# Kernel optimization log

Hardware: AMD Instinct MI355X
Metric: run time of the kernel (lower is better)

The kernel has to match this reference:

```python
import jax, jax.numpy as jnp
import numpy as np

D_MODEL = 768
NUM_HEADS = 12
D_K = D_MODEL // NUM_HEADS


def setup_inputs() -> dict:
    key = jax.random.key(0)
    ks = jax.random.split(key, 11)
    B, L = 1, 4096
    s = 1.0 / np.sqrt(D_MODEL)
    return {
        "q": jax.random.normal(ks[0], (B, L, D_MODEL), jnp.float32),
        "k": jax.random.normal(ks[1], (B, L, D_MODEL), jnp.float32),
        "v": jax.random.normal(ks[2], (B, L, D_MODEL), jnp.float32),
        "Wq": jax.random.normal(ks[3], (D_MODEL, D_MODEL), jnp.float32) * s,
        "bq": jax.random.normal(ks[4], (D_MODEL,), jnp.float32) * s,
        "Wk": jax.random.normal(ks[5], (D_MODEL, D_MODEL), jnp.float32) * s,
        "bk": jax.random.normal(ks[6], (D_MODEL,), jnp.float32) * s,
        "Wv": jax.random.normal(ks[7], (D_MODEL, D_MODEL), jnp.float32) * s,
        "bv": jax.random.normal(ks[8], (D_MODEL,), jnp.float32) * s,
        "Wo": jax.random.normal(ks[9], (D_MODEL, D_MODEL), jnp.float32) * s,
        "bo": jax.random.normal(ks[10], (D_MODEL,), jnp.float32) * s,
    }


def reference(q, k, v, Wq, bq, Wk, bk, Wv, bv, Wo, bo):
    B, L, _ = q.shape
    # linear projections (torch Linear: x @ W.T + b)
    qp = q @ Wq.T + bq
    kp = k @ Wk.T + bk
    vp = v @ Wv.T + bv
    # split heads: (B, H, L, d_k)
    def split(x):
        return x.reshape(B, L, NUM_HEADS, D_K).transpose(0, 2, 1, 3)
    qh, kh, vh = split(qp), split(kp), split(vp)
    scale = 1.0 / jnp.sqrt(jnp.asarray(D_K, qh.dtype))
    scores = jnp.einsum("bhqd,bhkd->bhqk", qh, kh) * scale  # (B,H,L,L)
    weights = jax.nn.softmax(scores, axis=-1)
    out = jnp.einsum("bhqk,bhkd->bhqd", weights, vh)
    out = out.transpose(0, 2, 1, 3).reshape(B, L, D_MODEL)
    return out @ Wo.T + bo
```

## Files before the change

### kernel.cpp

```cpp
#include <hip/hip_runtime.h>
#include <stdint.h>
#include <math.h>

#define L_SEQ  4096
#define DMODEL 768
#define NHEADS 12
#define DKH    64
#define QSCALE 0.18033688011112042f

typedef _Float16 f16;
typedef __attribute__((ext_vector_type(8))) _Float16 half8;
typedef __attribute__((ext_vector_type(4))) _Float16 half4;
typedef __attribute__((ext_vector_type(4))) float f32x4;
typedef __attribute__((ext_vector_type(16))) float f32x16;
typedef __attribute__((ext_vector_type(4))) unsigned int uint4v;

#define MFMA16(a, b, c) __builtin_amdgcn_mfma_f32_16x16x32_f16(a, b, c, 0, 0, 0)
#define MFMA32(a, b, c) __builtin_amdgcn_mfma_f32_32x32x16_f16(a, b, c, 0, 0, 0)

#define NE ((size_t)L_SEQ * DMODEL)
#define WE ((size_t)DMODEL * DMODEL)

static __device__ __forceinline__ unsigned int pack2(float a, float b) {
  return __builtin_bit_cast(unsigned int, __builtin_amdgcn_cvt_pkrtz(a, b));
}

__global__ __launch_bounds__(256)
void cvt_all(const float* __restrict__ q, const float* __restrict__ k,
             const float* __restrict__ v, const float* __restrict__ Wq,
             const float* __restrict__ Wk, const float* __restrict__ Wv,
             const float* __restrict__ Wo, f16* __restrict__ x16,
             f16* __restrict__ w16)
{
  const size_t NE4 = NE / 4, WE4 = WE / 4;
  size_t i = (size_t)blockIdx.x * 256 + threadIdx.x;
  const float* srcs[7] = {q, k, v, Wq, Wk, Wv, Wo};
  f16* dsts[7] = {x16, x16 + NE, x16 + 2 * NE,
                  w16, w16 + WE, w16 + 2 * WE, w16 + 3 * WE};
  const size_t sz4[7] = {NE4, NE4, NE4, WE4, WE4, WE4, WE4};
  int r = 0; size_t off = i;
  while (off >= sz4[r]) { off -= sz4[r]; ++r; }
  float4 f = reinterpret_cast<const float4*>(srcs[r])[off];
  half4 h; h[0] = (f16)f.x; h[1] = (f16)f.y; h[2] = (f16)f.z; h[3] = (f16)f.w;
  reinterpret_cast<half4*>(dsts[r])[off] = h;
}

template<int KIND>
__global__ __launch_bounds__(256)
void gemm_big(const f16* __restrict__ Abase, const f16* __restrict__ Wbase,
              const float* __restrict__ bq, const float* __restrict__ bk,
              const float* __restrict__ bv,
              f16* __restrict__ Qp, f16* __restrict__ Kp, f16* __restrict__ VpT,
              float* __restrict__ Ofp)
{
  __shared__ f16 As[128][72];
  __shared__ f16 Bs[128][72];
  const int tid  = threadIdx.x;
  const int lane = tid & 63, wid = tid >> 6;
  const int l31  = lane & 31, hc = lane >> 5;
  const int wm   = (wid & 1) * 64, wn = (wid >> 1) * 64;
  const int m0   = blockIdx.y * 128;

  int widx, n0;
  const f16 *A, *W;
  if (KIND == 0) {
    widx = blockIdx.x / 6;
    n0   = (blockIdx.x % 6) * 128;
    A = Abase + (size_t)widx * NE;
    W = Wbase + (size_t)widx * WE;
  } else {
    widx = 3;
    n0   = blockIdx.x * 128;
    A = Abase;
    W = Wbase;
  }

  const int srow = tid >> 1, sseg = (tid & 1) * 32;
  const f16* aptr = A + (size_t)(m0 + srow) * DMODEL + sseg;
  const f16* bptr = W + (size_t)(n0 + srow) * DMODEL + sseg;

  half8 ar[4], br[4];
#pragma unroll
  for (int t = 0; t < 4; ++t) {
    ar[t] = *reinterpret_cast<const half8*>(aptr + t * 8);
    br[t] = *reinterpret_cast<const half8*>(bptr + t * 8);
  }

  f32x16 acc[2][2] = {};

  for (int k0 = 0; k0 < DMODEL; k0 += 64) {
#pragma unroll
    for (int t = 0; t < 4; ++t) {
      *reinterpret_cast<half8*>(&As[srow][sseg + t * 8]) = ar[t];
      *reinterpret_cast<half8*>(&Bs[srow][sseg + t * 8]) = br[t];
    }
    __syncthreads();

    if (k0 + 64 < DMODEL) {
#pragma unroll
      for (int t = 0; t < 4; ++t) {
        ar[t] = *reinterpret_cast<const half8*>(aptr + k0 + 64 + t * 8);
        br[t] = *reinterpret_cast<const half8*>(bptr + k0 + 64 + t * 8);
      }
    }

#pragma unroll
    for (int s = 0; s < 4; ++s) {
      half8 af[2], bf[2];
#pragma unroll
      for (int a = 0; a < 2; ++a)
        af[a] = *reinterpret_cast<half8*>(&As[wm + a * 32 + l31][s * 16 + hc * 8]);
#pragma unroll
      for (int b = 0; b < 2; ++b)
        bf[b] = *reinterpret_cast<half8*>(&Bs[wn + b * 32 + l31][s * 16 + hc * 8]);
#pragma unroll
      for (int a = 0; a < 2; ++a)
#pragma unroll
        for (int b = 0; b < 2; ++b)
          acc[a][b] = MFMA32(af[a], bf[b], acc[a][b]);
    }
    __syncthreads();
  }

#pragma unroll
  for (int b = 0; b < 2; ++b) {
    const int gn = n0 + wn + b * 32 + l31;
    float bias;
    if (KIND == 0) bias = (widx == 0) ? bq[gn] : (widx == 1) ? bk[gn] : bv[gn];
    else           bias = bq[gn];
#pragma unroll
    for (int a = 0; a < 2; ++a) {
      const int gmb = m0 + wm + a * 32 + 4 * hc;
      if (KIND == 1) {
#pragma unroll
        for (int r = 0; r < 16; ++r) {
          const int gm = gmb + (r & 3) + 8 * (r >> 2);
          Ofp[(size_t)gm * DMODEL + gn] = acc[a][b][r] + bias;
        }
      } else if (widx == 2) {
#pragma unroll
        for (int g = 0; g < 4; ++g) {
          half4 o4;
#pragma unroll
          for (int t = 0; t < 4; ++t) o4[t] = (f16)(acc[a][b][4 * g + t] + bias);
          *reinterpret_cast<half4*>(VpT + (size_t)gn * L_SEQ + gmb + 8 * g) = o4;
        }
      } else if (widx == 0) {
#pragma unroll
        for (int r = 0; r < 16; ++r) {
          const int gm = gmb + (r & 3) + 8 * (r >> 2);
          Qp[(size_t)gm * DMODEL + gn] = (f16)((acc[a][b][r] + bias) * QSCALE);
        }
      } else {
#pragma unroll
        for (int r = 0; r < 16; ++r) {
          const int gm = gmb + (r & 3) + 8 * (r >> 2);
          Kp[(size_t)gm * DMODEL + gn] = (f16)(acc[a][b][r] + bias);
        }
      }
    }
  }
}

__global__ __launch_bounds__(256, 3)
void attn_mfma4(const f16* __restrict__ Qp, const f16* __restrict__ Kp,
                const f16* __restrict__ VpT, f16* __restrict__ AO)
{
  const int h  = blockIdx.x;
  const int q0 = blockIdx.y * 64;
  const int tid  = threadIdx.x;
  const int lane = tid & 63, wid = tid >> 6;
  const int l31  = lane & 31, hc = lane >> 5;
  const int qh   = wid & 1, kh = wid >> 1;

  __shared__ __align__(16) char smem[25088];
  f16 (*Ks)[72] = (f16 (*)[72])smem;
  f16 (*Vt)[72] = (f16 (*)[72])(smem + 9216);
  float* Of  = (float*)smem;
  float* lf  = (float*)(smem + 16384);
  f16*   Of16 = (f16*)(smem + 16640);

  half8 qf[4];
#pragma unroll
  for (int st = 0; st < 4; ++st)
    qf[st] = *reinterpret_cast<const half8*>(
        Qp + (size_t)(q0 + qh * 32 + l31) * DMODEL + h * DKH + st * 16 + hc * 8);

  f32x16 oacc[2] = {};
  float lsum = 0.0f;

  const int srow = tid >> 2, sseg = (tid & 3) * 16;
  const f16* kbase = Kp  + (size_t)srow * DMODEL + h * DKH + sseg;
  const f16* vbase = VpT + (size_t)(h * DKH + srow) * L_SEQ + sseg;

  half8 k0 = *reinterpret_cast<const half8*>(kbase);
  half8 k1 = *reinterpret_cast<const half8*>(kbase + 8);
  half8 v0 = *reinterpret_cast<const half8*>(vbase);
  half8 v1 = *reinterpret_cast<const half8*>(vbase + 8);

  for (int kt = 0; kt < L_SEQ; kt += 64) {
    *reinterpret_cast<half8*>(&Ks[srow][sseg])     = k0;
    *reinterpret_cast<half8*>(&Ks[srow][sseg + 8]) = k1;
    *reinterpret_cast<half8*>(&Vt[srow][sseg])     = v0;
    *reinterpret_cast<half8*>(&Vt[srow][sseg + 8]) = v1;
    __syncthreads();

    if (kt + 64 < L_SEQ) {
      const f16* kn = kbase + (size_t)(kt + 64) * DMODEL;
      const f16* vn = vbase + (kt + 64);
      k0 = *reinterpret_cast<const half8*>(kn);
      k1 = *reinterpret_cast<const half8*>(kn + 8);
      v0 = *reinterpret_cast<const half8*>(vn);
      v1 = *reinterpret_cast<const half8*>(vn + 8);
    }

    f32x16 s = {};
#pragma unroll
    for (int st = 0; st < 4; ++st) {
      half8 kf = *reinterpret_cast<half8*>(&Ks[kh * 32 + l31][st * 16 + hc * 8]);
      s = MFMA32(kf, qf[st], s);
    }

    unsigned int pk[8];
#pragma unroll
    for (int i = 0; i < 8; ++i) {
      float p0 = exp2f(s[2 * i]);
      float p1 = exp2f(s[2 * i + 1]);
      lsum += p0 + p1;
      pk[i] = pack2(p0, p1);
    }

    unsigned int recv[4];
#pragma unroll
    for (int j = 0; j < 4; ++j) {
      unsigned int sv = hc ? pk[(j & 1) + 4 * (j >> 1)]
                           : pk[2 + (j & 1) + 4 * (j >> 1)];
      recv[j] = (unsigned int)__shfl_xor((int)sv, 32);
    }

#pragma unroll
    for (int st = 0; st < 2; ++st) {
      uint4v pw;
#pragma unroll
      for (int t = 0; t < 4; ++t) {
        unsigned int h0v = (t < 2) ? pk[(t & 1) + 4 * st] : recv[2 * st + (t & 1)];
        unsigned int h1v = (t < 2) ? recv[2 * st + (t & 1)] : pk[(t & 1) + 4 * st + 2];
        pw[t] = hc ? h1v : h0v;
      }
      half8 pf = __builtin_bit_cast(half8, pw);
#pragma unroll
      for (int a = 0; a < 2; ++a) {
        half8 vf = *reinterpret_cast<half8*>(&Vt[a * 32 + l31][kh * 32 + st * 16 + hc * 8]);
        oacc[a] = MFMA32(vf, pf, oacc[a]);
      }
    }
    __syncthreads();
  }

  float lw = lsum + __shfl_xor(lsum, 32);

  if (kh == 0) {
#pragma unroll
    for (int a = 0; a < 2; ++a)
#pragma unroll
      for (int r = 0; r < 16; ++r) {
        int d = a * 32 + (r & 3) + 8 * (r >> 2) + 4 * hc;
        Of[((qh * 64) + d) * 32 + l31] = oacc[a][r];
      }
    if (lane < 32) lf[qh * 32 + l31] = lw;
  }
  __syncthreads();
  if (kh == 1) {
    const float inv = 1.0f / (lf[qh * 32 + l31] + lw);
#pragma unroll
    for (int a = 0; a < 2; ++a)
#pragma unroll
      for (int r = 0; r < 16; ++r) {
        int d = a * 32 + (r & 3) + 8 * (r >> 2) + 4 * hc;
        float val = (Of[((qh * 64) + d) * 32 + l31] + oacc[a][r]) * inv;
        Of16[(qh * 32 + l31) * 64 + d] = (f16)val;
      }
  }
  __syncthreads();

  *reinterpret_cast<half8*>(AO + (size_t)(q0 + srow) * DMODEL + h * DKH + sseg) =
      *reinterpret_cast<half8*>(&Of16[srow * 64 + sseg]);
  *reinterpret_cast<half8*>(AO + (size_t)(q0 + srow) * DMODEL + h * DKH + sseg + 8) =
      *reinterpret_cast<half8*>(&Of16[srow * 64 + sseg + 8]);
}

extern "C" void kernel_launch(void* const* d_in, const int* in_sizes, int n_in,
                              void* d_out, int out_size, void* d_ws, size_t ws_size,
                              hipStream_t stream) {
  const float* q  = (const float*)d_in[0];
  const float* k  = (const float*)d_in[1];
  const float* v  = (const float*)d_in[2];
  const float* Wq = (const float*)d_in[3];
  const float* bq = (const float*)d_in[4];
  const float* Wk = (const float*)d_in[5];
  const float* bk = (const float*)d_in[6];
  const float* Wv = (const float*)d_in[7];
  const float* bv = (const float*)d_in[8];
  const float* Wo = (const float*)d_in[9];
  const float* bo = (const float*)d_in[10];
  float* out = (float*)d_out;

  f16* x16 = (f16*)d_ws;
  f16* w16 = x16 + 3 * NE;
  f16* Qp  = w16 + 4 * WE;
  f16* Kp  = Qp + NE;
  f16* VpT = Kp + NE;
  f16* AO  = VpT + NE;

  const int ncvt = (int)((3 * (NE / 4) + 4 * (WE / 4)) / 256);
  cvt_all<<<ncvt, 256, 0, stream>>>(q, k, v, Wq, Wk, Wv, Wo, x16, w16);

  dim3 gqkv(18, L_SEQ / 128);
  gemm_big<0><<<gqkv, 256, 0, stream>>>(x16, w16, bq, bk, bv,
                                        Qp, Kp, VpT, nullptr);

  dim3 gattn(NHEADS, L_SEQ / 64);
  attn_mfma4<<<gattn, 256, 0, stream>>>(Qp, Kp, VpT, AO);

  dim3 gout(DMODEL / 128, L_SEQ / 128);
  gemm_big<1><<<gout, 256, 0, stream>>>(AO, w16 + 3 * WE, bo, nullptr, nullptr,
                                        nullptr, nullptr, nullptr, out);
}
```

Measured before the change: 249.0 us.

## Split attention keys across four waves and halve GEMM M-tile

The attention kernel grows to 512 threads with 8 waves, so each pair of query waves splits every 128-key tile four ways. Partial outputs and row sums are reduced serially through shared memory. The projection GEMMs use 64x128 tiles instead of 128x128, which doubles the block count for better CU occupancy. The trade-offs are extra reduction sync phases, more shared memory per attention block, and less operand reuse per GEMM block.

Measured after the change: 459.6 us. 84.6% more time.

```diff
diff --git a/kernel.cpp b/kernel.cpp
--- a/kernel.cpp
+++ b/kernel.cpp
@@ -11,11 +11,9 @@
 typedef _Float16 f16;
 typedef __attribute__((ext_vector_type(8))) _Float16 half8;
 typedef __attribute__((ext_vector_type(4))) _Float16 half4;
-typedef __attribute__((ext_vector_type(4))) float f32x4;
 typedef __attribute__((ext_vector_type(16))) float f32x16;
 typedef __attribute__((ext_vector_type(4))) unsigned int uint4v;
 
-#define MFMA16(a, b, c) __builtin_amdgcn_mfma_f32_16x16x32_f16(a, b, c, 0, 0, 0)
 #define MFMA32(a, b, c) __builtin_amdgcn_mfma_f32_32x32x16_f16(a, b, c, 0, 0, 0)
 
 #define NE ((size_t)L_SEQ * DMODEL)
@@ -47,19 +45,19 @@
 
 template<int KIND>
 __global__ __launch_bounds__(256)
-void gemm_big(const f16* __restrict__ Abase, const f16* __restrict__ Wbase,
-              const float* __restrict__ bq, const float* __restrict__ bk,
-              const float* __restrict__ bv,
-              f16* __restrict__ Qp, f16* __restrict__ Kp, f16* __restrict__ VpT,
-              float* __restrict__ Ofp)
+void gemm_t(const f16* __restrict__ Abase, const f16* __restrict__ Wbase,
+            const float* __restrict__ bq, const float* __restrict__ bk,
+            const float* __restrict__ bv,
+            f16* __restrict__ Qp, f16* __restrict__ Kp, f16* __restrict__ VpT,
+            float* __restrict__ Ofp)
 {
-  __shared__ f16 As[128][72];
+  __shared__ f16 As[64][72];
   __shared__ f16 Bs[128][72];
   const int tid  = threadIdx.x;
   const int lane = tid & 63, wid = tid >> 6;
   const int l31  = lane & 31, hc = lane >> 5;
-  const int wm   = (wid & 1) * 64, wn = (wid >> 1) * 64;
-  const int m0   = blockIdx.y * 128;
+  const int wm   = (wid & 1) * 32, wn = (wid >> 1) * 64;
+  const int m0   = blockIdx.y * 64;
 
   int widx, n0;
   const f16 *A, *W;
@@ -75,49 +73,47 @@
     W = Wbase;
   }
 
-  const int srow = tid >> 1, sseg = (tid & 1) * 32;
-  const f16* aptr = A + (size_t)(m0 + srow) * DMODEL + sseg;
-  const f16* bptr = W + (size_t)(n0 + srow) * DMODEL + sseg;
-
-  half8 ar[4], br[4];
-#pragma unroll
-  for (int t = 0; t < 4; ++t) {
-    ar[t] = *reinterpret_cast<const half8*>(aptr + t * 8);
-    br[t] = *reinterpret_cast<const half8*>(bptr + t * 8);
-  }
-
-  f32x16 acc[2][2] = {};
+  const int arow = tid >> 2, aseg = (tid & 3) * 16;
+  const int brow = tid >> 1, bseg = (tid & 1) * 32;
+  const f16* aptr = A + (size_t)(m0 + arow) * DMODEL + aseg;
+  const f16* bptr = W + (size_t)(n0 + brow) * DMODEL + bseg;
+
+  half8 ar[2], br[4];
+#pragma unroll
+  for (int t = 0; t < 2; ++t) ar[t] = *reinterpret_cast<const half8*>(aptr + t * 8);
+#pragma unroll
+  for (int t = 0; t < 4; ++t) br[t] = *reinterpret_cast<const half8*>(bptr + t * 8);
+
+  f32x16 acc[2] = {};
 
   for (int k0 = 0; k0 < DMODEL; k0 += 64) {
 #pragma unroll
-    for (int t = 0; t < 4; ++t) {
-      *reinterpret_cast<half8*>(&As[srow][sseg + t * 8]) = ar[t];
-      *reinterpret_cast<half8*>(&Bs[srow][sseg + t * 8]) = br[t];
-    }
+    for (int t = 0; t < 2; ++t)
+      *reinterpret_cast<half8*>(&As[arow][aseg + t * 8]) = ar[t];
+#pragma unroll
+    for (int t = 0; t < 4; ++t)
+      *reinterpret_cast<half8*>(&Bs[brow][bseg + t * 8]) = br[t];
     __syncthreads();
 
     if (k0 + 64 < DMODEL) {
 #pragma unroll
-      for (int t = 0; t < 4; ++t) {
+      for (int t = 0; t < 2; ++t)
         ar[t] = *reinterpret_cast<const half8*>(aptr + k0 + 64 + t * 8);
+#pragma unroll
+      for (int t = 0; t < 4; ++t)
         br[t] = *reinterpret_cast<const half8*>(bptr + k0 + 64 + t * 8);
-      }
     }
 
 #pragma unroll
     for (int s = 0; s < 4; ++s) {
-      half8 af[2], bf[2];
-#pragma unroll
-      for (int a = 0; a < 2; ++a)
-        af[a] = *reinterpret_cast<half8*>(&As[wm + a * 32 + l31][s * 16 + hc * 8]);
+      half8 af = *reinterpret_cast<half8*>(&As[wm + l31][s * 16 + hc * 8]);
+      half8 bf[2];
 #pragma unroll
       for (int b = 0; b < 2; ++b)
         bf[b] = *reinterpret_cast<half8*>(&Bs[wn + b * 32 + l31][s * 16 + hc * 8]);
 #pragma unroll
-      for (int a = 0; a < 2; ++a)
-#pragma unroll
-        for (int b = 0; b < 2; ++b)
-          acc[a][b] = MFMA32(af[a], bf[b], acc[a][b]);
+      for (int b = 0; b < 2; ++b)
+        acc[b] = MFMA32(af, bf[b], acc[b]);
     }
     __syncthreads();
   }
@@ -128,42 +124,39 @@
     float bias;
     if (KIND == 0) bias = (widx == 0) ? bq[gn] : (widx == 1) ? bk[gn] : bv[gn];
     else           bias = bq[gn];
-#pragma unroll
-    for (int a = 0; a < 2; ++a) {
-      const int gmb = m0 + wm + a * 32 + 4 * hc;
-      if (KIND == 1) {
-#pragma unroll
-        for (int r = 0; r < 16; ++r) {
-          const int gm = gmb + (r & 3) + 8 * (r >> 2);
-          Ofp[(size_t)gm * DMODEL + gn] = acc[a][b][r] + bias;
-        }
-      } else if (widx == 2) {
-#pragma unroll
-        for (int g = 0; g < 4; ++g) {
-          half4 o4;
-#pragma unroll
-          for (int t = 0; t < 4; ++t) o4[t] = (f16)(acc[a][b][4 * g + t] + bias);
-          *reinterpret_cast<half4*>(VpT + (size_t)gn * L_SEQ + gmb + 8 * g) = o4;
-        }
-      } else if (widx == 0) {
-#pragma unroll
-        for (int r = 0; r < 16; ++r) {
-          const int gm = gmb + (r & 3) + 8 * (r >> 2);
-          Qp[(size_t)gm * DMODEL + gn] = (f16)((acc[a][b][r] + bias) * QSCALE);
-        }
-      } else {
-#pragma unroll
-        for (int r = 0; r < 16; ++r) {
-          const int gm = gmb + (r & 3) + 8 * (r >> 2);
-          Kp[(size_t)gm * DMODEL + gn] = (f16)(acc[a][b][r] + bias);
-        }
-      }
-    }
-  }
-}
-
-__global__ __launch_bounds__(256, 3)
-void attn_mfma4(const f16* __restrict__ Qp, const f16* __restrict__ Kp,
+    const int gmb = m0 + wm + 4 * hc;
+    if (KIND == 1) {
+#pragma unroll
+      for (int r = 0; r < 16; ++r) {
+        const int gm = gmb + (r & 3) + 8 * (r >> 2);
+        Ofp[(size_t)gm * DMODEL + gn] = acc[b][r] + bias;
+      }
+    } else if (widx == 2) {
+#pragma unroll
+      for (int g = 0; g < 4; ++g) {
+        half4 o4;
+#pragma unroll
+        for (int t = 0; t < 4; ++t) o4[t] = (f16)(acc[b][4 * g + t] + bias);
+        *reinterpret_cast<half4*>(VpT + (size_t)gn * L_SEQ + gmb + 8 * g) = o4;
+      }
+    } else if (widx == 0) {
+#pragma unroll
+      for (int r = 0; r < 16; ++r) {
+        const int gm = gmb + (r & 3) + 8 * (r >> 2);
+        Qp[(size_t)gm * DMODEL + gn] = (f16)((acc[b][r] + bias) * QSCALE);
+      }
+    } else {
+#pragma unroll
+      for (int r = 0; r < 16; ++r) {
+        const int gm = gmb + (r & 3) + 8 * (r >> 2);
+        Kp[(size_t)gm * DMODEL + gn] = (f16)(acc[b][r] + bias);
+      }
+    }
+  }
+}
+
+__global__ __launch_bounds__(512, 6)
+void attn_mfma5(const f16* __restrict__ Qp, const f16* __restrict__ Kp,
                 const f16* __restrict__ VpT, f16* __restrict__ AO)
 {
   const int h  = blockIdx.x;
@@ -171,13 +164,13 @@
   const int tid  = threadIdx.x;
   const int lane = tid & 63, wid = tid >> 6;
   const int l31  = lane & 31, hc = lane >> 5;
-  const int qh   = wid & 1, kh = wid >> 1;
-
-  __shared__ __align__(16) char smem[25088];
-  f16 (*Ks)[72] = (f16 (*)[72])smem;
-  f16 (*Vt)[72] = (f16 (*)[72])(smem + 9216);
-  float* Of  = (float*)smem;
-  float* lf  = (float*)(smem + 16384);
+  const int qh   = wid & 1, kq = wid >> 1;
+
+  __shared__ __align__(16) char smem[35840];
+  f16 (*Ks)[72]  = (f16 (*)[72])smem;
+  f16 (*Vt)[136] = (f16 (*)[136])(smem + 18432);
+  float* Of   = (float*)smem;
+  float* lf   = (float*)(smem + 16384);
   f16*   Of16 = (f16*)(smem + 16640);
 
   half8 qf[4];
@@ -189,25 +182,26 @@
   f32x16 oacc[2] = {};
   float lsum = 0.0f;
 
-  const int srow = tid >> 2, sseg = (tid & 3) * 16;
-  const f16* kbase = Kp  + (size_t)srow * DMODEL + h * DKH + sseg;
-  const f16* vbase = VpT + (size_t)(h * DKH + srow) * L_SEQ + sseg;
+  const int krow = tid >> 2, kseg = (tid & 3) * 16;
+  const int vrow = tid >> 3, vseg = (tid & 7) * 16;
+  const f16* kbase = Kp  + (size_t)krow * DMODEL + h * DKH + kseg;
+  const f16* vbase = VpT + (size_t)(h * DKH + vrow) * L_SEQ + vseg;
 
   half8 k0 = *reinterpret_cast<const half8*>(kbase);
   half8 k1 = *reinterpret_cast<const half8*>(kbase + 8);
   half8 v0 = *reinterpret_cast<const half8*>(vbase);
   half8 v1 = *reinterpret_cast<const half8*>(vbase + 8);
 
-  for (int kt = 0; kt < L_SEQ; kt += 64) {
-    *reinterpret_cast<half8*>(&Ks[srow][sseg])     = k0;
-    *reinterpret_cast<half8*>(&Ks[srow][sseg + 8]) = k1;
-    *reinterpret_cast<half8*>(&Vt[srow][sseg])     = v0;
-    *reinterpret_cast<half8*>(&Vt[srow][sseg + 8]) = v1;
-    __syncthreads();
-
-    if (kt + 64 < L_SEQ) {
-      const f16* kn = kbase + (size_t)(kt + 64) * DMODEL;
-      const f16* vn = vbase + (kt + 64);
+  for (int kt = 0; kt < L_SEQ; kt += 128) {
+    *reinterpret_cast<half8*>(&Ks[krow][kseg])     = k0;
+    *reinterpret_cast<half8*>(&Ks[krow][kseg + 8]) = k1;
+    *reinterpret_cast<half8*>(&Vt[vrow][vseg])     = v0;
+    *reinterpret_cast<half8*>(&Vt[vrow][vseg + 8]) = v1;
+    __syncthreads();
+
+    if (kt + 128 < L_SEQ) {
+      const f16* kn = kbase + (size_t)(kt + 128) * DMODEL;
+      const f16* vn = vbase + (kt + 128);
       k0 = *reinterpret_cast<const half8*>(kn);
       k1 = *reinterpret_cast<const half8*>(kn + 8);
       v0 = *reinterpret_cast<const half8*>(vn);
@@ -217,7 +211,7 @@
     f32x16 s = {};
 #pragma unroll
     for (int st = 0; st < 4; ++st) {
-      half8 kf = *reinterpret_cast<half8*>(&Ks[kh * 32 + l31][st * 16 + hc * 8]);
+      half8 kf = *reinterpret_cast<half8*>(&Ks[kq * 32 + l31][st * 16 + hc * 8]);
       s = MFMA32(kf, qf[st], s);
     }
 
@@ -250,7 +244,8 @@
       half8 pf = __builtin_bit_cast(half8, pw);
 #pragma unroll
       for (int a = 0; a < 2; ++a) {
-        half8 vf = *reinterpret_cast<half8*>(&Vt[a * 32 + l31][kh * 32 + st * 16 + hc * 8]);
+        half8 vf = *reinterpret_cast<half8*>(
+            &Vt[a * 32 + l31][kq * 32 + st * 16 + hc * 8]);
         oacc[a] = MFMA32(vf, pf, oacc[a]);
       }
     }
@@ -259,7 +254,7 @@
 
   float lw = lsum + __shfl_xor(lsum, 32);
 
-  if (kh == 0) {
+  if (kq == 0) {
 #pragma unroll
     for (int a = 0; a < 2; ++a)
 #pragma unroll
@@ -270,7 +265,21 @@
     if (lane < 32) lf[qh * 32 + l31] = lw;
   }
   __syncthreads();
-  if (kh == 1) {
+#pragma unroll
+  for (int ph = 1; ph < 3; ++ph) {
+    if (kq == ph) {
+#pragma unroll
+      for (int a = 0; a < 2; ++a)
+#pragma unroll
+        for (int r = 0; r < 16; ++r) {
+          int d = a * 32 + (r & 3) + 8 * (r >> 2) + 4 * hc;
+          Of[((qh * 64) + d) * 32 + l31] += oacc[a][r];
+        }
+      if (lane < 32) lf[qh * 32 + l31] += lw;
+    }
+    __syncthreads();
+  }
+  if (kq == 3) {
     const float inv = 1.0f / (lf[qh * 32 + l31] + lw);
 #pragma unroll
     for (int a = 0; a < 2; ++a)
@@ -283,10 +292,9 @@
   }
   __syncthreads();
 
-  *reinterpret_cast<half8*>(AO + (size_t)(q0 + srow) * DMODEL + h * DKH + sseg) =
-      *reinterpret_cast<half8*>(&Of16[srow * 64 + sseg]);
-  *reinterpret_cast<half8*>(AO + (size_t)(q0 + srow) * DMODEL + h * DKH + sseg + 8) =
-      *reinterpret_cast<half8*>(&Of16[srow * 64 + sseg + 8]);
+  const int orow = tid >> 3, oseg = (tid & 7) * 8;
+  *reinterpret_cast<half8*>(AO + (size_t)(q0 + orow) * DMODEL + h * DKH + oseg) =
+      *reinterpret_cast<half8*>(&Of16[orow * 64 + oseg]);
 }
 
 extern "C" void kernel_launch(void* const* d_in, const int* in_sizes, int n_in,
@@ -315,14 +323,14 @@
   const int ncvt = (int)((3 * (NE / 4) + 4 * (WE / 4)) / 256);
   cvt_all<<<ncvt, 256, 0, stream>>>(q, k, v, Wq, Wk, Wv, Wo, x16, w16);
 
-  dim3 gqkv(18, L_SEQ / 128);
-  gemm_big<0><<<gqkv, 256, 0, stream>>>(x16, w16, bq, bk, bv,
-                                        Qp, Kp, VpT, nullptr);
+  dim3 gqkv(18, L_SEQ / 64);
+  gemm_t<0><<<gqkv, 256, 0, stream>>>(x16, w16, bq, bk, bv,
+                                      Qp, Kp, VpT, nullptr);
 
   dim3 gattn(NHEADS, L_SEQ / 64);
-  attn_mfma4<<<gattn, 256, 0, stream>>>(Qp, Kp, VpT, AO);
-
-  dim3 gout(DMODEL / 128, L_SEQ / 128);
-  gemm_big<1><<<gout, 256, 0, stream>>>(AO, w16 + 3 * WE, bo, nullptr, nullptr,
-                                        nullptr, nullptr, nullptr, out);
-}
+  attn_mfma5<<<gattn, 512, 0, stream>>>(Qp, Kp, VpT, AO);
+
+  dim3 gout(DMODEL / 128, L_SEQ / 64);
+  gemm_t<1><<<gout, 256, 0, stream>>>(AO, w16 + 3 * WE, bo, nullptr, nullptr,
+                                      nullptr, nullptr, nullptr, out);
+}
```
